# Optimization experiments

Hardware: AMD Instinct MI355X
Metric: run time of the kernel (lower is better)

The kernel has to match this reference:

```python
import math
import jax, jax.numpy as jnp
import numpy as np

B, T, C = 2, 2048, 1024
HEADS = 16
HD = C // HEADS  # 64


def setup_inputs() -> dict:
    key = jax.random.key(0)
    ks = jax.random.split(key, 5)
    s = 0.02
    return {
        "x": jax.random.normal(ks[0], (B, T, C), jnp.float32),
        "Wq": jax.random.normal(ks[1], (C, C), jnp.float32) * s,
        "bq": jnp.zeros((C,), jnp.float32),
        "Wk": jax.random.normal(ks[2], (C, HD), jnp.float32) * s,
        "bk": jnp.zeros((HD,), jnp.float32),
        "Wv": jax.random.normal(ks[3], (C, HD), jnp.float32) * s,
        "bv": jnp.zeros((HD,), jnp.float32),
        "Wo": jax.random.normal(ks[4], (C, C), jnp.float32) * s,
        "bo": jnp.zeros((C,), jnp.float32),
    }


def _rope_tables(seq_len, dim):
    pos = jnp.arange(seq_len, dtype=jnp.float32)
    freqs = 1.0 / (10000.0 ** (jnp.arange(0, dim, 2, dtype=jnp.float32) / dim))
    ang = pos[:, None] * freqs[None, :]          # (T, dim//2)
    # broadcast over (B, T, H, dim//2)
    return jnp.sin(ang)[None, :, None, :], jnp.cos(ang)[None, :, None, :]


def _apply_rope(t, sin, cos, dim):
    t1, t2 = t[..., : dim // 2], t[..., dim // 2 :]
    # matches torch source: emb[..., :d/2]=sin, emb[..., d/2:]=cos
    return jnp.concatenate([t1 * cos + t2 * sin, t1 * sin - t2 * cos], axis=-1)


def reference(x, Wq, bq, Wk, bk, Wv, bv, Wo, bo):
    Bx, Tx, Cx = x.shape
    q = (x @ Wq + bq).reshape(Bx, Tx, HEADS, HD)   # (B,T,H,hd)
    k = (x @ Wk + bk)[:, :, None, :]               # (B,T,1,hd) single KV head (MQA)
    v = (x @ Wv + bv)[:, :, None, :]
    sin, cos = _rope_tables(Tx, HD)
    q = _apply_rope(q, sin, cos, HD)
    k = _apply_rope(k, sin, cos, HD)
    att = jnp.einsum('bthd,bThd->bhtT', q, k) / math.sqrt(HD)
    causal = jnp.triu(jnp.ones((Tx, Tx), bool), 1)
    att = jnp.where(causal, -jnp.inf, att)
    att = jax.nn.softmax(att, axis=-1)
    out = jnp.einsum('bhtT,bThd->bthd', att, v).reshape(Bx, Tx, Cx)
    return out @ Wo + bo
```

## Files before the change

kernel.cpp:

```cpp
#include <hip/hip_runtime.h>
#include <math.h>

#define BSZ   2
#define TSEQ  2048
#define CDIM  1024
#define NHEAD 16
#define HDIM  64
#define BT    (BSZ*TSEQ)
#define NQKV  1152

typedef __attribute__((ext_vector_type(8))) short short8;
typedef __attribute__((ext_vector_type(4))) float f32x4;
typedef unsigned short u16;
typedef unsigned int   u32;

__device__ __forceinline__ u16 f2b(float f) {
    union { float f; u32 u; } c; c.f = f;
    u32 u = c.u;
    u += 0x7fffu + ((u >> 16) & 1u);
    return (u16)(u >> 16);
}
__device__ __forceinline__ u32 pack2(float lo, float hi) {
    return (u32)f2b(lo) | ((u32)f2b(hi) << 16);
}

__device__ __forceinline__ void async_copy16(const void* g, void* l) {
    __builtin_amdgcn_global_load_lds(
        (__attribute__((address_space(1))) const void*)g,
        (__attribute__((address_space(3))) void*)l,
        16, 0, 0);
}

__device__ __forceinline__ void transpose_tile(
    const float* __restrict__ W, u16* __restrict__ Wt,
    int K, int Nw, int nofs, int bx, int by, float (*T)[65])
{
    const int tid = threadIdx.x;
    const int k0 = by * 64, n0 = bx * 64;
    #pragma unroll
    for (int i = 0; i < 16; ++i) {
        int idx = i * 256 + tid, r = idx >> 6, c = idx & 63;
        T[r][c] = W[(size_t)(k0 + r) * Nw + n0 + c];
    }
    __syncthreads();
    #pragma unroll
    for (int i = 0; i < 16; ++i) {
        int idx = i * 256 + tid, rn = idx >> 6, ck = idx & 63;
        Wt[(size_t)(nofs + n0 + rn) * K + k0 + ck] = f2b(T[ck][rn]);
    }
}

__global__ __launch_bounds__(256) void prep_kernel(
    const float* __restrict__ x,
    const float* __restrict__ Wq, const float* __restrict__ Wk,
    const float* __restrict__ Wv, const float* __restrict__ Wo,
    const float* __restrict__ bq, const float* __restrict__ bk,
    const float* __restrict__ bv,
    u16* __restrict__ xb,
    u16* __restrict__ Wqkvt, u16* __restrict__ Wot, float* __restrict__ bqkv)
{
    __shared__ float T[64][65];
    const int bid = blockIdx.x;
    if (bid < 4096) {
        int i = bid * 256 + threadIdx.x;
        float4 f = ((const float4*)x)[i];
        u16* d = xb + (size_t)i * 4;
        d[0] = f2b(f.x); d[1] = f2b(f.y); d[2] = f2b(f.z); d[3] = f2b(f.w);
    } else if (bid < 4352) {
        int b2 = bid - 4096;
        transpose_tile(Wq, Wqkvt, 1024, 1024, 0, b2 & 15, b2 >> 4, T);
    } else if (bid < 4368) {
        transpose_tile(Wk, Wqkvt, 1024, 64, 1024, 0, bid - 4352, T);
    } else if (bid < 4384) {
        transpose_tile(Wv, Wqkvt, 1024, 64, 1088, 0, bid - 4368, T);
    } else if (bid < 4640) {
        int b2 = bid - 4384;
        transpose_tile(Wo, Wot, 1024, 1024, 0, b2 & 15, b2 >> 4, T);
    } else {
        for (int i = threadIdx.x; i < NQKV; i += 256)
            bqkv[i] = (i < 1024) ? bq[i] : (i < 1088 ? bk[i - 1024] : bv[i - 1088]);
    }
}

__global__ __launch_bounds__(256) void gemm_qkv_kernel(
    const u16* __restrict__ A, const u16* __restrict__ Bt,
    const float* __restrict__ bias,
    u16* __restrict__ qb, u16* __restrict__ kb, u16* __restrict__ vT)
{
    __shared__ __align__(16) u16 AsC[64 * 32];
    __shared__ __align__(16) u16 BsC[128 * 32];
    const int tid  = threadIdx.x;
    const int wave = tid >> 6, lane = tid & 63;
    const int ln16 = lane & 15, quad = lane >> 4;
    const int wm = wave >> 1, wn = wave & 1;
    const int m0 = blockIdx.y * 64, n0 = blockIdx.x * 128;
    const int K = CDIM;

    const int c_row = ((tid >> 6) << 4) + (tid & 15);
    const int c_k   = ((tid >> 4) & 3) * 8;
    const u16* ag  = &A [(size_t)(m0 + c_row)       * K + c_k];
    const u16* bg0 = &Bt[(size_t)(n0 + c_row)       * K + c_k];
    const u16* bg1 = &Bt[(size_t)(n0 + 64 + c_row)  * K + c_k];
    u16* a_l  = &AsC[(size_t)wave * 64 * 8];
    u16* b_l0 = &BsC[(size_t)wave * 64 * 8];
    u16* b_l1 = &BsC[(size_t)(wave + 4) * 64 * 8];

    f32x4 acc[2][4];
    #pragma unroll
    for (int i = 0; i < 2; ++i)
        #pragma unroll
        for (int j = 0; j < 4; ++j) acc[i][j] = (f32x4){0.f, 0.f, 0.f, 0.f};

    for (int k0 = 0; k0 < K; k0 += 32) {
        async_copy16(ag,  a_l);
        async_copy16(bg0, b_l0);
        async_copy16(bg1, b_l1);
        ag += 32; bg0 += 32; bg1 += 32;
        __syncthreads();

        short8 af[2], bf[4];
        #pragma unroll
        for (int mt = 0; mt < 2; ++mt)
            af[mt] = *(const short8*)&AsC[(((wm * 2 + mt) * 64) + quad * 16 + ln16) * 8];
        #pragma unroll
        for (int nt = 0; nt < 4; ++nt)
            bf[nt] = *(const short8*)&BsC[(((wn * 4 + nt) * 64) + quad * 16 + ln16) * 8];
        #pragma unroll
        for (int mt = 0; mt < 2; ++mt)
            #pragma unroll
            for (int nt = 0; nt < 4; ++nt)
                acc[mt][nt] = __builtin_amdgcn_mfma_f32_16x16x32_bf16(
                    af[mt], bf[nt], acc[mt][nt], 0, 0, 0);
        __syncthreads();
    }

    #pragma unroll
    for (int mt = 0; mt < 2; ++mt)
        #pragma unroll
        for (int nt = 0; nt < 4; ++nt) {
            float bb = bias[n0 + wn * 64 + nt * 16 + ln16];
            #pragma unroll
            for (int r = 0; r < 4; ++r) acc[mt][nt][r] += bb;
        }

    const int col0 = n0 + wn * 64;
    if (col0 < 1024) {
        const int hh = col0 >> 6;
        #pragma unroll
        for (int nt = 0; nt < 2; ++nt) {
            int j = nt * 16 + ln16;
            float fr = exp2f(-0.41524101186092029f * (float)j);
            #pragma unroll
            for (int mt = 0; mt < 2; ++mt)
                #pragma unroll
                for (int r = 0; r < 4; ++r) {
                    int m = m0 + wm * 32 + mt * 16 + quad * 4 + r;
                    float sn, cs;
                    __sincosf((float)(m & (TSEQ - 1)) * fr, &sn, &cs);
                    float t1 = acc[mt][nt][r], t2 = acc[mt][nt + 2][r];
                    u16* o = qb + (size_t)m * CDIM + hh * 64 + j;
                    o[0]  = f2b(fmaf(t1, cs,  t2 * sn) * 0.18033688011112043f);
                    o[32] = f2b(fmaf(t1, sn, -t2 * cs) * 0.18033688011112043f);
                }
        }
    } else if (wn == 0) {
        #pragma unroll
        for (int nt = 0; nt < 2; ++nt) {
            int j = nt * 16 + ln16;
            float fr = exp2f(-0.41524101186092029f * (float)j);
            #pragma unroll
            for (int mt = 0; mt < 2; ++mt)
                #pragma unroll
                for (int r = 0; r < 4; ++r) {
                    int m = m0 + wm * 32 + mt * 16 + quad * 4 + r;
                    float sn, cs;
                    __sincosf((float)(m & (TSEQ - 1)) * fr, &sn, &cs);
                    float t1 = acc[mt][nt][r], t2 = acc[mt][nt + 2][r];
                    u16* o = kb + (size_t)m * HDIM + j;
                    o[0]  = f2b(fmaf(t1, cs,  t2 * sn));
                    o[32] = f2b(fmaf(t1, sn, -t2 * cs));
                }
        }
    } else {
        #pragma unroll
        for (int nt = 0; nt < 4; ++nt) {
            int d = nt * 16 + ln16;
            #pragma unroll
            for (int mt = 0; mt < 2; ++mt) {
                int mr = m0 + wm * 32 + mt * 16 + quad * 4;
                int b  = mr >> 11, tq = mr & (TSEQ - 1);
                uint2 val;
                val.x = pack2(acc[mt][nt][0], acc[mt][nt][1]);
                val.y = pack2(acc[mt][nt][2], acc[mt][nt][3]);
                *(uint2*)&vT[(size_t)(b * HDIM + d) * TSEQ + tq] = val;
            }
        }
    }
}

__global__ __launch_bounds__(256) void gemm_mfma_kernel(
    const u16* __restrict__ A, const u16* __restrict__ Bt,
    const float* __restrict__ bias, float* __restrict__ Y,
    int M, int N, int K)
{
    __shared__ __align__(16) u16 AsC[64 * 32];
    __shared__ __align__(16) u16 BsC[128 * 32];
    const int tid  = threadIdx.x;
    const int wave = tid >> 6, lane = tid & 63;
    const int ln16 = lane & 15, quad = lane >> 4;
    const int wm = wave >> 1, wn = wave & 1;
    const int m0 = blockIdx.y * 64, n0 = blockIdx.x * 128;

    const int c_row = ((tid >> 6) << 4) + (tid & 15);
    const int c_k   = ((tid >> 4) & 3) * 8;
    const u16* ag  = &A [(size_t)(m0 + c_row)       * K + c_k];
    const u16* bg0 = &Bt[(size_t)(n0 + c_row)       * K + c_k];
    const u16* bg1 = &Bt[(size_t)(n0 + 64 + c_row)  * K + c_k];
    u16* a_l  = &AsC[(size_t)wave * 64 * 8];
    u16* b_l0 = &BsC[(size_t)wave * 64 * 8];
    u16* b_l1 = &BsC[(size_t)(wave + 4) * 64 * 8];

    f32x4 acc[2][4];
    #pragma unroll
    for (int i = 0; i < 2; ++i)
        #pragma unroll
        for (int j = 0; j < 4; ++j) acc[i][j] = (f32x4){0.f, 0.f, 0.f, 0.f};

    for (int k0 = 0; k0 < K; k0 += 32) {
        async_copy16(ag,  a_l);
        async_copy16(bg0, b_l0);
        async_copy16(bg1, b_l1);
        ag += 32; bg0 += 32; bg1 += 32;
        __syncthreads();

        short8 af[2], bf[4];
        #pragma unroll
        for (int mt = 0; mt < 2; ++mt)
            af[mt] = *(const short8*)&AsC[(((wm * 2 + mt) * 64) + quad * 16 + ln16) * 8];
        #pragma unroll
        for (int nt = 0; nt < 4; ++nt)
            bf[nt] = *(const short8*)&BsC[(((wn * 4 + nt) * 64) + quad * 16 + ln16) * 8];
        #pragma unroll
        for (int mt = 0; mt < 2; ++mt)
            #pragma unroll
            for (int nt = 0; nt < 4; ++nt)
                acc[mt][nt] = __builtin_amdgcn_mfma_f32_16x16x32_bf16(
                    af[mt], bf[nt], acc[mt][nt], 0, 0, 0);
        __syncthreads();
    }

    #pragma unroll
    for (int mt = 0; mt < 2; ++mt)
        #pragma unroll
        for (int nt = 0; nt < 4; ++nt) {
            int n = n0 + wn * 64 + nt * 16 + ln16;
            float bb = bias[n];
            #pragma unroll
            for (int r = 0; r < 4; ++r) {
                int m = m0 + wm * 32 + mt * 16 + quad * 4 + r;
                Y[(size_t)m * N + n] = acc[mt][nt][r] + bb;
            }
        }
}

__device__ __forceinline__ void flash_stage_kv(
    const u16* __restrict__ kb, const u16* __restrict__ vT,
    int b, int kt, u16* __restrict__ Ksb, u16* __restrict__ Vsb,
    const int* row_c, const int* off_c, int c0)
{
    const size_t kt0 = (size_t)(b * TSEQ + kt * 64);
    #pragma unroll
    for (int hf = 0; hf < 2; ++hf) {
        int cc = c0 + hf * 256;
        async_copy16(kb + (kt0 + row_c[hf]) * HDIM + off_c[hf], Ksb + cc * 8);
        async_copy16(vT + (size_t)(b * HDIM + row_c[hf]) * TSEQ + kt * 64 + off_c[hf],
                     Vsb + cc * 8);
    }
}

__device__ __forceinline__ void flash_tile(
    const u16* __restrict__ Ksb, const u16* __restrict__ Vsb,
    const u16* __restrict__ Qs, u16* __restrict__ Pw,
    int wave, int ln16, int quad, bool diag,
    float* lsum, f32x4* oacc)
{
    f32x4 sv[4];
    #pragma unroll
    for (int t = 0; t < 4; ++t) sv[t] = (f32x4){0.f, 0.f, 0.f, 0.f};
    #pragma unroll
    for (int kk2 = 0; kk2 < 2; ++kk2) {
        short8 af = *(const short8*)&Qs[(wave * 128 + kk2 * 64 + quad * 16 + ln16) * 8];
        #pragma unroll
        for (int t = 0; t < 4; ++t) {
            short8 bf = *(const short8*)&Ksb[(t * 128 + kk2 * 64 + quad * 16 + ln16) * 8];
            sv[t] = __builtin_amdgcn_mfma_f32_16x16x32_bf16(af, bf, sv[t], 0, 0, 0);
        }
    }

    if (diag) {
        #pragma unroll
        for (int t = 0; t < 4; ++t) {
            int key = t * 16 + ln16;
            #pragma unroll
            for (int r = 0; r < 4; ++r) {
                float e = (key > wave * 16 + quad * 4 + r) ? 0.f : exp2f(sv[t][r]);
                u32 bits = __float_as_uint(e);
                lsum[r] += __uint_as_float(bits & 0xffff0000u);
                Pw[(quad * 4 + r) * 72 + t * 16 + ln16] = (u16)(bits >> 16);
            }
        }
    } else {
        #pragma unroll
        for (int t = 0; t < 4; ++t)
            #pragma unroll
            for (int r = 0; r < 4; ++r) {
                float e = exp2f(sv[t][r]);
                u32 bits = __float_as_uint(e);
                lsum[r] += __uint_as_float(bits & 0xffff0000u);
                Pw[(quad * 4 + r) * 72 + t * 16 + ln16] = (u16)(bits >> 16);
            }
    }

    #pragma unroll
    for (int kk2 = 0; kk2 < 2; ++kk2) {
        short8 pf = *(const short8*)&Pw[ln16 * 72 + kk2 * 32 + quad * 8];
        #pragma unroll
        for (int t = 0; t < 4; ++t) {
            short8 vf = *(const short8*)&Vsb[(t * 128 + kk2 * 64 + quad * 16 + ln16) * 8];
            oacc[t] = __builtin_amdgcn_mfma_f32_16x16x32_bf16(pf, vf, oacc[t], 0, 0, 0);
        }
    }
}

__global__ __launch_bounds__(256) void flash_mfma_kernel(
    const u16* __restrict__ qb, const u16* __restrict__ kb,
    const u16* __restrict__ vT, u16* __restrict__ o)
{
    const int id  = blockIdx.x;
    const int qt  = 31 - (id >> 5);
    const int hb  = id & 31;
    const int h   = hb >> 1;
    const int b   = hb & 1;
    __shared__ __align__(16) u16 Qs [512 * 8];
    __shared__ __align__(16) u16 Ks0[512 * 8];
    __shared__ __align__(16) u16 Ks1[512 * 8];
    __shared__ __align__(16) u16 Vs0[512 * 8];
    __shared__ __align__(16) u16 Vs1[512 * 8];
    __shared__ __align__(16) u16 Ps[4 * 16 * 72];

    const int tid  = threadIdx.x;
    const int wave = tid >> 6, lane = tid & 63;
    const int ln16 = lane & 15, quad = lane >> 4;

    const int c0 = tid;
    int row_c[2], off_c[2];
    #pragma unroll
    for (int hf = 0; hf < 2; ++hf) {
        int c = c0 + hf * 256;
        row_c[hf] = ((c >> 7) << 4) | (c & 15);
        off_c[hf] = ((c >> 6) & 1) * 32 + ((c >> 4) & 3) * 8;
    }

    u16* Pw = &Ps[wave * 16 * 72];

    #pragma unroll
    for (int hf = 0; hf < 2; ++hf)
        async_copy16(
            qb + (size_t)(b * TSEQ + qt * 64 + row_c[hf]) * CDIM + h * HDIM + off_c[hf],
            Qs + (c0 + hf * 256) * 8);
    flash_stage_kv(kb, vT, b, 0, Ks0, Vs0, row_c, off_c, c0);

    float lsum[4];
    f32x4 oacc[4];
    #pragma unroll
    for (int r = 0; r < 4; ++r) lsum[r] = 0.f;
    #pragma unroll
    for (int t = 0; t < 4; ++t) oacc[t] = (f32x4){0.f, 0.f, 0.f, 0.f};

    int kt = 0;
    while (true) {
        __syncthreads();
        if (kt < qt) flash_stage_kv(kb, vT, b, kt + 1, Ks1, Vs1, row_c, off_c, c0);
        flash_tile(Ks0, Vs0, Qs, Pw, wave, ln16, quad, kt == qt, lsum, oacc);
        if (++kt > qt) break;
        __syncthreads();
        if (kt < qt) flash_stage_kv(kb, vT, b, kt + 1, Ks0, Vs0, row_c, off_c, c0);
        flash_tile(Ks1, Vs1, Qs, Pw, wave, ln16, quad, kt == qt, lsum, oacc);
        if (++kt > qt) break;
    }

    float inv[4];
    #pragma unroll
    for (int r = 0; r < 4; ++r) {
        float l = lsum[r];
        #pragma unroll
        for (int off = 1; off < 16; off <<= 1)
            l += __shfl_xor(l, off, 64);
        inv[r] = 1.0f / l;
    }
    #pragma unroll
    for (int t = 0; t < 4; ++t) {
        #pragma unroll
        for (int r = 0; r < 4; ++r) {
            int row = qt * 64 + wave * 16 + quad * 4 + r;
            int d   = t * 16 + ln16;
            o[(size_t)(b * TSEQ + row) * CDIM + h * HDIM + d] = f2b(oacc[t][r] * inv[r]);
        }
    }
}

extern "C" void kernel_launch(void* const* d_in, const int* in_sizes, int n_in,
                              void* d_out, int out_size, void* d_ws, size_t ws_size,
                              hipStream_t stream)
{
    const float* x  = (const float*)d_in[0];
    const float* Wq = (const float*)d_in[1];
    const float* bq = (const float*)d_in[2];
    const float* Wk = (const float*)d_in[3];
    const float* bk = (const float*)d_in[4];
    const float* Wv = (const float*)d_in[5];
    const float* bv = (const float*)d_in[6];
    const float* Wo = (const float*)d_in[7];
    const float* bo = (const float*)d_in[8];
    float* out = (float*)d_out;

    const size_t MB = 1u << 20;
    char* w = (char*)d_ws;
    u16*   xb   = (u16*)(w);
    u16*   aob  = (u16*)(w);
    u16*   qb   = (u16*)(w + 8 * MB);
    u16*   kb   = (u16*)(w + 16 * MB);
    u16*   vT   = (u16*)(w + 16 * MB + 512 * 1024);
    u16*   Wqkvt= (u16*)(w + 17 * MB);
    u16*   Wot  = (u16*)(w + 20 * MB);
    float* bqkv = (float*)(w + 22 * MB);

    prep_kernel<<<dim3(4641), dim3(256), 0, stream>>>(
        x, Wq, Wk, Wv, Wo, bq, bk, bv, xb, Wqkvt, Wot, bqkv);
    gemm_qkv_kernel<<<dim3(NQKV / 128, BT / 64), dim3(256), 0, stream>>>(
        xb, Wqkvt, bqkv, qb, kb, vT);
    flash_mfma_kernel<<<dim3(32 * NHEAD * BSZ), dim3(256), 0, stream>>>(
        qb, kb, vT, aob);
    gemm_mfma_kernel<<<dim3(CDIM / 128, BT / 64), dim3(256), 0, stream>>>(
        aob, Wot, bo, out, BT, CDIM, CDIM);
}
```

Before: 192.5 us.

## Enlarge GEMM tiles to 128x128 and pair causal query tiles per flash block

Both GEMM kernels now compute 128x128 output tiles per block, with each wave holding a 64x64 accumulator, which halves the grid and increases operand reuse from shared memory. The flash attention kernel now processes two query tiles per block, pid and 31-pid, so every block does the same amount of causal work and the grid is halved. The aim is better data reuse in the GEMMs and better load balance in attention. In exchange the GEMMs use more registers and run fewer blocks (288 and 256), which may leave the 256 CUs of the MI355X under-occupied, and attention now launches only 512 blocks.

```diff
diff --git a/kernel.cpp b/kernel.cpp
--- a/kernel.cpp
+++ b/kernel.cpp
@@ -87,46 +87,49 @@
     const float* __restrict__ bias,
     u16* __restrict__ qb, u16* __restrict__ kb, u16* __restrict__ vT)
 {
-    __shared__ __align__(16) u16 AsC[64 * 32];
+    __shared__ __align__(16) u16 AsC[128 * 32];
     __shared__ __align__(16) u16 BsC[128 * 32];
     const int tid  = threadIdx.x;
     const int wave = tid >> 6, lane = tid & 63;
     const int ln16 = lane & 15, quad = lane >> 4;
     const int wm = wave >> 1, wn = wave & 1;
-    const int m0 = blockIdx.y * 64, n0 = blockIdx.x * 128;
+    const int m0 = blockIdx.y * 128, n0 = blockIdx.x * 128;
     const int K = CDIM;
 
-    const int c_row = ((tid >> 6) << 4) + (tid & 15);
-    const int c_k   = ((tid >> 4) & 3) * 8;
-    const u16* ag  = &A [(size_t)(m0 + c_row)       * K + c_k];
+    const int c_row = (wave << 4) + ln16;
+    const int c_k   = quad * 8;
+    const u16* ag0 = &A [(size_t)(m0 + c_row)       * K + c_k];
+    const u16* ag1 = &A [(size_t)(m0 + 64 + c_row)  * K + c_k];
     const u16* bg0 = &Bt[(size_t)(n0 + c_row)       * K + c_k];
     const u16* bg1 = &Bt[(size_t)(n0 + 64 + c_row)  * K + c_k];
-    u16* a_l  = &AsC[(size_t)wave * 64 * 8];
+    u16* a_l0 = &AsC[(size_t)wave * 64 * 8];
+    u16* a_l1 = &AsC[(size_t)(wave + 4) * 64 * 8];
     u16* b_l0 = &BsC[(size_t)wave * 64 * 8];
     u16* b_l1 = &BsC[(size_t)(wave + 4) * 64 * 8];
 
-    f32x4 acc[2][4];
-    #pragma unroll
-    for (int i = 0; i < 2; ++i)
+    f32x4 acc[4][4];
+    #pragma unroll
+    for (int i = 0; i < 4; ++i)
         #pragma unroll
         for (int j = 0; j < 4; ++j) acc[i][j] = (f32x4){0.f, 0.f, 0.f, 0.f};
 
     for (int k0 = 0; k0 < K; k0 += 32) {
-        async_copy16(ag,  a_l);
+        async_copy16(ag0, a_l0);
+        async_copy16(ag1, a_l1);
         async_copy16(bg0, b_l0);
         async_copy16(bg1, b_l1);
-        ag += 32; bg0 += 32; bg1 += 32;
+        ag0 += 32; ag1 += 32; bg0 += 32; bg1 += 32;
         __syncthreads();
 
-        short8 af[2], bf[4];
-        #pragma unroll
-        for (int mt = 0; mt < 2; ++mt)
-            af[mt] = *(const short8*)&AsC[(((wm * 2 + mt) * 64) + quad * 16 + ln16) * 8];
+        short8 af[4], bf[4];
+        #pragma unroll
+        for (int mt = 0; mt < 4; ++mt)
+            af[mt] = *(const short8*)&AsC[(((wm * 4 + mt) * 64) + quad * 16 + ln16) * 8];
         #pragma unroll
         for (int nt = 0; nt < 4; ++nt)
             bf[nt] = *(const short8*)&BsC[(((wn * 4 + nt) * 64) + quad * 16 + ln16) * 8];
         #pragma unroll
-        for (int mt = 0; mt < 2; ++mt)
+        for (int mt = 0; mt < 4; ++mt)
             #pragma unroll
             for (int nt = 0; nt < 4; ++nt)
                 acc[mt][nt] = __builtin_amdgcn_mfma_f32_16x16x32_bf16(
@@ -135,7 +138,7 @@
     }
 
     #pragma unroll
-    for (int mt = 0; mt < 2; ++mt)
+    for (int mt = 0; mt < 4; ++mt)
         #pragma unroll
         for (int nt = 0; nt < 4; ++nt) {
             float bb = bias[n0 + wn * 64 + nt * 16 + ln16];
@@ -151,10 +154,10 @@
             int j = nt * 16 + ln16;
             float fr = exp2f(-0.41524101186092029f * (float)j);
             #pragma unroll
-            for (int mt = 0; mt < 2; ++mt)
+            for (int mt = 0; mt < 4; ++mt)
                 #pragma unroll
                 for (int r = 0; r < 4; ++r) {
-                    int m = m0 + wm * 32 + mt * 16 + quad * 4 + r;
+                    int m = m0 + wm * 64 + mt * 16 + quad * 4 + r;
                     float sn, cs;
                     __sincosf((float)(m & (TSEQ - 1)) * fr, &sn, &cs);
                     float t1 = acc[mt][nt][r], t2 = acc[mt][nt + 2][r];
@@ -169,10 +172,10 @@
             int j = nt * 16 + ln16;
             float fr = exp2f(-0.41524101186092029f * (float)j);
             #pragma unroll
-            for (int mt = 0; mt < 2; ++mt)
+            for (int mt = 0; mt < 4; ++mt)
                 #pragma unroll
                 for (int r = 0; r < 4; ++r) {
-                    int m = m0 + wm * 32 + mt * 16 + quad * 4 + r;
+                    int m = m0 + wm * 64 + mt * 16 + quad * 4 + r;
                     float sn, cs;
                     __sincosf((float)(m & (TSEQ - 1)) * fr, &sn, &cs);
                     float t1 = acc[mt][nt][r], t2 = acc[mt][nt + 2][r];
@@ -186,8 +189,8 @@
         for (int nt = 0; nt < 4; ++nt) {
             int d = nt * 16 + ln16;
             #pragma unroll
-            for (int mt = 0; mt < 2; ++mt) {
-                int mr = m0 + wm * 32 + mt * 16 + quad * 4;
+            for (int mt = 0; mt < 4; ++mt) {
+                int mr = m0 + wm * 64 + mt * 16 + quad * 4;
                 int b  = mr >> 11, tq = mr & (TSEQ - 1);
                 uint2 val;
                 val.x = pack2(acc[mt][nt][0], acc[mt][nt][1]);
@@ -203,45 +206,48 @@
     const float* __restrict__ bias, float* __restrict__ Y,
     int M, int N, int K)
 {
-    __shared__ __align__(16) u16 AsC[64 * 32];
+    __shared__ __align__(16) u16 AsC[128 * 32];
     __shared__ __align__(16) u16 BsC[128 * 32];
     const int tid  = threadIdx.x;
     const int wave = tid >> 6, lane = tid & 63;
     const int ln16 = lane & 15, quad = lane >> 4;
     const int wm = wave >> 1, wn = wave & 1;
-    const int m0 = blockIdx.y * 64, n0 = blockIdx.x * 128;
-
-    const int c_row = ((tid >> 6) << 4) + (tid & 15);
-    const int c_k   = ((tid >> 4) & 3) * 8;
-    const u16* ag  = &A [(size_t)(m0 + c_row)       * K + c_k];
+    const int m0 = blockIdx.y * 128, n0 = blockIdx.x * 128;
+
+    const int c_row = (wave << 4) + ln16;
+    const int c_k   = quad * 8;
+    const u16* ag0 = &A [(size_t)(m0 + c_row)       * K + c_k];
+    const u16* ag1 = &A [(size_t)(m0 + 64 + c_row)  * K + c_k];
     const u16* bg0 = &Bt[(size_t)(n0 + c_row)       * K + c_k];
     const u16* bg1 = &Bt[(size_t)(n0 + 64 + c_row)  * K + c_k];
-    u16* a_l  = &AsC[(size_t)wave * 64 * 8];
+    u16* a_l0 = &AsC[(size_t)wave * 64 * 8];
+    u16* a_l1 = &AsC[(size_t)(wave + 4) * 64 * 8];
     u16* b_l0 = &BsC[(size_t)wave * 64 * 8];
     u16* b_l1 = &BsC[(size_t)(wave + 4) * 64 * 8];
 
-    f32x4 acc[2][4];
-    #pragma unroll
-    for (int i = 0; i < 2; ++i)
+    f32x4 acc[4][4];
+    #pragma unroll
+    for (int i = 0; i < 4; ++i)
         #pragma unroll
         for (int j = 0; j < 4; ++j) acc[i][j] = (f32x4){0.f, 0.f, 0.f, 0.f};
 
     for (int k0 = 0; k0 < K; k0 += 32) {
-        async_copy16(ag,  a_l);
+        async_copy16(ag0, a_l0);
+        async_copy16(ag1, a_l1);
         async_copy16(bg0, b_l0);
         async_copy16(bg1, b_l1);
-        ag += 32; bg0 += 32; bg1 += 32;
+        ag0 += 32; ag1 += 32; bg0 += 32; bg1 += 32;
         __syncthreads();
 
-        short8 af[2], bf[4];
-        #pragma unroll
-        for (int mt = 0; mt < 2; ++mt)
-            af[mt] = *(const short8*)&AsC[(((wm * 2 + mt) * 64) + quad * 16 + ln16) * 8];
+        short8 af[4], bf[4];
+        #pragma unroll
+        for (int mt = 0; mt < 4; ++mt)
+            af[mt] = *(const short8*)&AsC[(((wm * 4 + mt) * 64) + quad * 16 + ln16) * 8];
         #pragma unroll
         for (int nt = 0; nt < 4; ++nt)
             bf[nt] = *(const short8*)&BsC[(((wn * 4 + nt) * 64) + quad * 16 + ln16) * 8];
         #pragma unroll
-        for (int mt = 0; mt < 2; ++mt)
+        for (int mt = 0; mt < 4; ++mt)
             #pragma unroll
             for (int nt = 0; nt < 4; ++nt)
                 acc[mt][nt] = __builtin_amdgcn_mfma_f32_16x16x32_bf16(
@@ -250,14 +256,14 @@
     }
 
     #pragma unroll
-    for (int mt = 0; mt < 2; ++mt)
+    for (int mt = 0; mt < 4; ++mt)
         #pragma unroll
         for (int nt = 0; nt < 4; ++nt) {
             int n = n0 + wn * 64 + nt * 16 + ln16;
             float bb = bias[n];
             #pragma unroll
             for (int r = 0; r < 4; ++r) {
-                int m = m0 + wm * 32 + mt * 16 + quad * 4 + r;
+                int m = m0 + wm * 64 + mt * 16 + quad * 4 + r;
                 Y[(size_t)m * N + n] = acc[mt][nt][r] + bb;
             }
         }
@@ -337,7 +343,7 @@
     const u16* __restrict__ vT, u16* __restrict__ o)
 {
     const int id  = blockIdx.x;
-    const int qt  = 31 - (id >> 5);
+    const int pid = id >> 5;
     const int hb  = id & 31;
     const int h   = hb >> 1;
     const int b   = hb & 1;
@@ -363,48 +369,54 @@
 
     u16* Pw = &Ps[wave * 16 * 72];
 
-    #pragma unroll
-    for (int hf = 0; hf < 2; ++hf)
-        async_copy16(
-            qb + (size_t)(b * TSEQ + qt * 64 + row_c[hf]) * CDIM + h * HDIM + off_c[hf],
-            Qs + (c0 + hf * 256) * 8);
-    flash_stage_kv(kb, vT, b, 0, Ks0, Vs0, row_c, off_c, c0);
-
-    float lsum[4];
-    f32x4 oacc[4];
-    #pragma unroll
-    for (int r = 0; r < 4; ++r) lsum[r] = 0.f;
-    #pragma unroll
-    for (int t = 0; t < 4; ++t) oacc[t] = (f32x4){0.f, 0.f, 0.f, 0.f};
-
-    int kt = 0;
-    while (true) {
-        __syncthreads();
-        if (kt < qt) flash_stage_kv(kb, vT, b, kt + 1, Ks1, Vs1, row_c, off_c, c0);
-        flash_tile(Ks0, Vs0, Qs, Pw, wave, ln16, quad, kt == qt, lsum, oacc);
-        if (++kt > qt) break;
-        __syncthreads();
-        if (kt < qt) flash_stage_kv(kb, vT, b, kt + 1, Ks0, Vs0, row_c, off_c, c0);
-        flash_tile(Ks1, Vs1, Qs, Pw, wave, ln16, quad, kt == qt, lsum, oacc);
-        if (++kt > qt) break;
-    }
-
-    float inv[4];
-    #pragma unroll
-    for (int r = 0; r < 4; ++r) {
-        float l = lsum[r];
-        #pragma unroll
-        for (int off = 1; off < 16; off <<= 1)
-            l += __shfl_xor(l, off, 64);
-        inv[r] = 1.0f / l;
-    }
-    #pragma unroll
-    for (int t = 0; t < 4; ++t) {
+    #pragma unroll 1
+    for (int ph = 0; ph < 2; ++ph) {
+        const int qt = ph ? (31 - pid) : pid;
+        if (ph) __syncthreads();
+
+        #pragma unroll
+        for (int hf = 0; hf < 2; ++hf)
+            async_copy16(
+                qb + (size_t)(b * TSEQ + qt * 64 + row_c[hf]) * CDIM + h * HDIM + off_c[hf],
+                Qs + (c0 + hf * 256) * 8);
+        flash_stage_kv(kb, vT, b, 0, Ks0, Vs0, row_c, off_c, c0);
+
+        float lsum[4];
+        f32x4 oacc[4];
+        #pragma unroll
+        for (int r = 0; r < 4; ++r) lsum[r] = 0.f;
+        #pragma unroll
+        for (int t = 0; t < 4; ++t) oacc[t] = (f32x4){0.f, 0.f, 0.f, 0.f};
+
+        int kt = 0;
+        while (true) {
+            __syncthreads();
+            if (kt < qt) flash_stage_kv(kb, vT, b, kt + 1, Ks1, Vs1, row_c, off_c, c0);
+            flash_tile(Ks0, Vs0, Qs, Pw, wave, ln16, quad, kt == qt, lsum, oacc);
+            if (++kt > qt) break;
+            __syncthreads();
+            if (kt < qt) flash_stage_kv(kb, vT, b, kt + 1, Ks0, Vs0, row_c, off_c, c0);
+            flash_tile(Ks1, Vs1, Qs, Pw, wave, ln16, quad, kt == qt, lsum, oacc);
+            if (++kt > qt) break;
+        }
+
+        float inv[4];
         #pragma unroll
         for (int r = 0; r < 4; ++r) {
-            int row = qt * 64 + wave * 16 + quad * 4 + r;
-            int d   = t * 16 + ln16;
-            o[(size_t)(b * TSEQ + row) * CDIM + h * HDIM + d] = f2b(oacc[t][r] * inv[r]);
+            float l = lsum[r];
+            #pragma unroll
+            for (int off = 1; off < 16; off <<= 1)
+                l += __shfl_xor(l, off, 64);
+            inv[r] = 1.0f / l;
+        }
+        #pragma unroll
+        for (int t = 0; t < 4; ++t) {
+            #pragma unroll
+            for (int r = 0; r < 4; ++r) {
+                int row = qt * 64 + wave * 16 + quad * 4 + r;
+                int d   = t * 16 + ln16;
+                o[(size_t)(b * TSEQ + row) * CDIM + h * HDIM + d] = f2b(oacc[t][r] * inv[r]);
+            }
         }
     }
 }
@@ -437,10 +449,10 @@
 
     prep_kernel<<<dim3(4641), dim3(256), 0, stream>>>(
         x, Wq, Wk, Wv, Wo, bq, bk, bv, xb, Wqkvt, Wot, bqkv);
-    gemm_qkv_kernel<<<dim3(NQKV / 128, BT / 64), dim3(256), 0, stream>>>(
+    gemm_qkv_kernel<<<dim3(NQKV / 128, BT / 128), dim3(256), 0, stream>>>(
         xb, Wqkvt, bqkv, qb, kb, vT);
-    flash_mfma_kernel<<<dim3(32 * NHEAD * BSZ), dim3(256), 0, stream>>>(
+    flash_mfma_kernel<<<dim3(16 * NHEAD * BSZ), dim3(256), 0, stream>>>(
         qb, kb, vT, aob);
-    gemm_mfma_kernel<<<dim3(CDIM / 128, BT / 64), dim3(256), 0, stream>>>(
+    gemm_mfma_kernel<<<dim3(CDIM / 128, BT / 128), dim3(256), 0, stream>>>(
         aob, Wot, bo, out, BT, CDIM, CDIM);
 }
```

Result: slower. 202.7 us (+5.3%).

## Enlarge flash query tile to 128 rows, pair causal tiles, MFMA row sums

Applied to the files above, without the earlier changes.

The attention kernel now processes 128 query rows per block (32 per wave, two 16-row MFMA tiles), so each staged K/V tile is reused across twice as many queries. Each block handles a pair of query tiles (pr and 15-pr) in sequence to balance causal work, and the grid shrinks to 256 blocks. Row sums of P are now computed with an MFMA against a ones vector instead of scalar adds plus shuffles, and V fragments are kept in registers across both row tiles. This raises register pressure and LDS use, and the smaller grid may underfill the GPU's compute units.

```diff
diff --git a/kernel.cpp b/kernel.cpp
--- a/kernel.cpp
+++ b/kernel.cpp
@@ -278,56 +278,73 @@
     }
 }
 
-__device__ __forceinline__ void flash_tile(
+__device__ __forceinline__ void flash_tile128(
     const u16* __restrict__ Ksb, const u16* __restrict__ Vsb,
     const u16* __restrict__ Qs, u16* __restrict__ Pw,
-    int wave, int ln16, int quad, bool diag,
-    float* lsum, f32x4* oacc)
-{
-    f32x4 sv[4];
-    #pragma unroll
-    for (int t = 0; t < 4; ++t) sv[t] = (f32x4){0.f, 0.f, 0.f, 0.f};
+    int wave, int ln16, int quad, int rbase, int kbase,
+    f32x4* lacc, f32x4 (*oacc)[4])
+{
+    if (kbase >= rbase + 32) return;
+    const bool diag = (kbase + 63 > rbase);
+
+    f32x4 sv[2][4];
+    #pragma unroll
+    for (int mt = 0; mt < 2; ++mt)
+        #pragma unroll
+        for (int t = 0; t < 4; ++t) sv[mt][t] = (f32x4){0.f, 0.f, 0.f, 0.f};
     #pragma unroll
     for (int kk2 = 0; kk2 < 2; ++kk2) {
-        short8 af = *(const short8*)&Qs[(wave * 128 + kk2 * 64 + quad * 16 + ln16) * 8];
+        short8 af0 = *(const short8*)&Qs[((wave * 2 + 0) * 128 + kk2 * 64 + quad * 16 + ln16) * 8];
+        short8 af1 = *(const short8*)&Qs[((wave * 2 + 1) * 128 + kk2 * 64 + quad * 16 + ln16) * 8];
         #pragma unroll
         for (int t = 0; t < 4; ++t) {
             short8 bf = *(const short8*)&Ksb[(t * 128 + kk2 * 64 + quad * 16 + ln16) * 8];
-            sv[t] = __builtin_amdgcn_mfma_f32_16x16x32_bf16(af, bf, sv[t], 0, 0, 0);
-        }
-    }
-
-    if (diag) {
-        #pragma unroll
-        for (int t = 0; t < 4; ++t) {
-            int key = t * 16 + ln16;
-            #pragma unroll
-            for (int r = 0; r < 4; ++r) {
-                float e = (key > wave * 16 + quad * 4 + r) ? 0.f : exp2f(sv[t][r]);
-                u32 bits = __float_as_uint(e);
-                lsum[r] += __uint_as_float(bits & 0xffff0000u);
-                Pw[(quad * 4 + r) * 72 + t * 16 + ln16] = (u16)(bits >> 16);
+            sv[0][t] = __builtin_amdgcn_mfma_f32_16x16x32_bf16(af0, bf, sv[0][t], 0, 0, 0);
+            sv[1][t] = __builtin_amdgcn_mfma_f32_16x16x32_bf16(af1, bf, sv[1][t], 0, 0, 0);
+        }
+    }
+
+    const short8 ones = {0x3F80, 0x3F80, 0x3F80, 0x3F80,
+                         0x3F80, 0x3F80, 0x3F80, 0x3F80};
+    short8 vreg[8];
+
+    #pragma unroll
+    for (int mt = 0; mt < 2; ++mt) {
+        if (diag) {
+            #pragma unroll
+            for (int t = 0; t < 4; ++t) {
+                int key = kbase + t * 16 + ln16;
+                #pragma unroll
+                for (int r = 0; r < 4; ++r) {
+                    int row = rbase + mt * 16 + quad * 4 + r;
+                    float e = (key > row) ? 0.f : exp2f(sv[mt][t][r]);
+                    Pw[(quad * 4 + r) * 72 + t * 16 + ln16] =
+                        (u16)(__float_as_uint(e) >> 16);
+                }
             }
-        }
-    } else {
-        #pragma unroll
-        for (int t = 0; t < 4; ++t)
-            #pragma unroll
-            for (int r = 0; r < 4; ++r) {
-                float e = exp2f(sv[t][r]);
-                u32 bits = __float_as_uint(e);
-                lsum[r] += __uint_as_float(bits & 0xffff0000u);
-                Pw[(quad * 4 + r) * 72 + t * 16 + ln16] = (u16)(bits >> 16);
+        } else {
+            #pragma unroll
+            for (int t = 0; t < 4; ++t)
+                #pragma unroll
+                for (int r = 0; r < 4; ++r) {
+                    float e = exp2f(sv[mt][t][r]);
+                    Pw[(quad * 4 + r) * 72 + t * 16 + ln16] =
+                        (u16)(__float_as_uint(e) >> 16);
+                }
+        }
+
+        #pragma unroll
+        for (int kk2 = 0; kk2 < 2; ++kk2) {
+            short8 pf = *(const short8*)&Pw[ln16 * 72 + kk2 * 32 + quad * 8];
+            lacc[mt] = __builtin_amdgcn_mfma_f32_16x16x32_bf16(pf, ones, lacc[mt], 0, 0, 0);
+            #pragma unroll
+            for (int t = 0; t < 4; ++t) {
+                if (mt == 0)
+                    vreg[kk2 * 4 + t] =
+                        *(const short8*)&Vsb[(t * 128 + kk2 * 64 + quad * 16 + ln16) * 8];
+                oacc[mt][t] = __builtin_amdgcn_mfma_f32_16x16x32_bf16(
+                    pf, vreg[kk2 * 4 + t], oacc[mt][t], 0, 0, 0);
             }
-    }
-
-    #pragma unroll
-    for (int kk2 = 0; kk2 < 2; ++kk2) {
-        short8 pf = *(const short8*)&Pw[ln16 * 72 + kk2 * 32 + quad * 8];
-        #pragma unroll
-        for (int t = 0; t < 4; ++t) {
-            short8 vf = *(const short8*)&Vsb[(t * 128 + kk2 * 64 + quad * 16 + ln16) * 8];
-            oacc[t] = __builtin_amdgcn_mfma_f32_16x16x32_bf16(pf, vf, oacc[t], 0, 0, 0);
         }
     }
 }
@@ -337,11 +354,11 @@
     const u16* __restrict__ vT, u16* __restrict__ o)
 {
     const int id  = blockIdx.x;
-    const int qt  = 31 - (id >> 5);
+    const int pr  = id >> 5;
     const int hb  = id & 31;
     const int h   = hb >> 1;
     const int b   = hb & 1;
-    __shared__ __align__(16) u16 Qs [512 * 8];
+    __shared__ __align__(16) u16 Qs [1024 * 8];
     __shared__ __align__(16) u16 Ks0[512 * 8];
     __shared__ __align__(16) u16 Ks1[512 * 8];
     __shared__ __align__(16) u16 Vs0[512 * 8];
@@ -363,49 +380,63 @@
 
     u16* Pw = &Ps[wave * 16 * 72];
 
-    #pragma unroll
-    for (int hf = 0; hf < 2; ++hf)
-        async_copy16(
-            qb + (size_t)(b * TSEQ + qt * 64 + row_c[hf]) * CDIM + h * HDIM + off_c[hf],
-            Qs + (c0 + hf * 256) * 8);
-    flash_stage_kv(kb, vT, b, 0, Ks0, Vs0, row_c, off_c, c0);
-
-    float lsum[4];
-    f32x4 oacc[4];
-    #pragma unroll
-    for (int r = 0; r < 4; ++r) lsum[r] = 0.f;
-    #pragma unroll
-    for (int t = 0; t < 4; ++t) oacc[t] = (f32x4){0.f, 0.f, 0.f, 0.f};
-
-    int kt = 0;
-    while (true) {
-        __syncthreads();
-        if (kt < qt) flash_stage_kv(kb, vT, b, kt + 1, Ks1, Vs1, row_c, off_c, c0);
-        flash_tile(Ks0, Vs0, Qs, Pw, wave, ln16, quad, kt == qt, lsum, oacc);
-        if (++kt > qt) break;
-        __syncthreads();
-        if (kt < qt) flash_stage_kv(kb, vT, b, kt + 1, Ks0, Vs0, row_c, off_c, c0);
-        flash_tile(Ks1, Vs1, Qs, Pw, wave, ln16, quad, kt == qt, lsum, oacc);
-        if (++kt > qt) break;
-    }
-
-    float inv[4];
-    #pragma unroll
-    for (int r = 0; r < 4; ++r) {
-        float l = lsum[r];
-        #pragma unroll
-        for (int off = 1; off < 16; off <<= 1)
-            l += __shfl_xor(l, off, 64);
-        inv[r] = 1.0f / l;
-    }
-    #pragma unroll
-    for (int t = 0; t < 4; ++t) {
+    #pragma unroll 1
+    for (int ph = 0; ph < 2; ++ph) {
+        const int qt = ph ? (15 - pr) : pr;
+        const int nt = 2 * qt + 2;
+        if (ph) __syncthreads();
+
+        #pragma unroll
+        for (int cc = 0; cc < 4; ++cc) {
+            int c  = c0 + cc * 256;
+            int rw = ((c >> 7) << 4) | (c & 15);
+            int of = ((c >> 6) & 1) * 32 + ((c >> 4) & 3) * 8;
+            async_copy16(
+                qb + (size_t)(b * TSEQ + qt * 128 + rw) * CDIM + h * HDIM + of,
+                Qs + (size_t)c * 8);
+        }
+        flash_stage_kv(kb, vT, b, 0, Ks0, Vs0, row_c, off_c, c0);
+
+        f32x4 lacc[2];
+        f32x4 oacc[2][4];
+        #pragma unroll
+        for (int mt = 0; mt < 2; ++mt) {
+            lacc[mt] = (f32x4){0.f, 0.f, 0.f, 0.f};
+            #pragma unroll
+            for (int t = 0; t < 4; ++t) oacc[mt][t] = (f32x4){0.f, 0.f, 0.f, 0.f};
+        }
+
+        const int rbase = qt * 128 + wave * 32;
+
+        int kt = 0;
+        while (true) {
+            __syncthreads();
+            if (kt + 1 < nt) flash_stage_kv(kb, vT, b, kt + 1, Ks1, Vs1, row_c, off_c, c0);
+            flash_tile128(Ks0, Vs0, Qs, Pw, wave, ln16, quad, rbase, kt * 64, lacc, oacc);
+            if (++kt >= nt) break;
+            __syncthreads();
+            if (kt + 1 < nt) flash_stage_kv(kb, vT, b, kt + 1, Ks0, Vs0, row_c, off_c, c0);
+            flash_tile128(Ks1, Vs1, Qs, Pw, wave, ln16, quad, rbase, kt * 64, lacc, oacc);
+            if (++kt >= nt) break;
+        }
+
+        float inv0[4], inv1[4];
         #pragma unroll
         for (int r = 0; r < 4; ++r) {
-            int row = qt * 64 + wave * 16 + quad * 4 + r;
-            int d   = t * 16 + ln16;
-            o[(size_t)(b * TSEQ + row) * CDIM + h * HDIM + d] = f2b(oacc[t][r] * inv[r]);
-        }
+            inv0[r] = 1.0f / lacc[0][r];
+            inv1[r] = 1.0f / lacc[1][r];
+        }
+        #pragma unroll
+        for (int mt = 0; mt < 2; ++mt)
+            #pragma unroll
+            for (int t = 0; t < 4; ++t)
+                #pragma unroll
+                for (int r = 0; r < 4; ++r) {
+                    int row = rbase + mt * 16 + quad * 4 + r;
+                    int d   = t * 16 + ln16;
+                    o[(size_t)(b * TSEQ + row) * CDIM + h * HDIM + d] =
+                        f2b(oacc[mt][t][r] * (mt ? inv1[r] : inv0[r]));
+                }
     }
 }
 
@@ -439,7 +470,7 @@
         x, Wq, Wk, Wv, Wo, bq, bk, bv, xb, Wqkvt, Wot, bqkv);
     gemm_qkv_kernel<<<dim3(NQKV / 128, BT / 64), dim3(256), 0, stream>>>(
         xb, Wqkvt, bqkv, qb, kb, vT);
-    flash_mfma_kernel<<<dim3(32 * NHEAD * BSZ), dim3(256), 0, stream>>>(
+    flash_mfma_kernel<<<dim3(8 * NHEAD * BSZ), dim3(256), 0, stream>>>(
         qb, kb, vT, aob);
     gemm_mfma_kernel<<<dim3(CDIM / 128, BT / 64), dim3(256), 0, stream>>>(
         aob, Wot, bo, out, BT, CDIM, CDIM);
```

Result: slower. 207.8 us (+7.9%).

## Double-buffer GEMM LDS tiles and compute softmax row sums via MFMA

Applied to the files above, without the earlier changes.

Both GEMM kernels switch to two LDS buffers, so the async copy of the next K-slice is issued before the MFMA work on the current slice, removing one barrier per step. The flash kernel stops accumulating per-lane row sums with scalar adds and shuffle reductions. It instead multiplies the bf16 P tile by a ones vector through an extra MFMA, which gives the row sum directly. This adds LDS usage and one MFMA per half-tile, in exchange for fewer VALU ops and no final cross-lane reduction.

```diff
diff --git a/kernel.cpp b/kernel.cpp
--- a/kernel.cpp
+++ b/kernel.cpp
@@ -82,13 +82,32 @@
     }
 }
 
+__device__ __forceinline__ void gemm_step(
+    const u16* __restrict__ As, const u16* __restrict__ Bs,
+    int wm, int wn, int quad, int ln16, f32x4 (*acc)[4])
+{
+    short8 af[2], bf[4];
+    #pragma unroll
+    for (int mt = 0; mt < 2; ++mt)
+        af[mt] = *(const short8*)&As[(((wm * 2 + mt) * 64) + quad * 16 + ln16) * 8];
+    #pragma unroll
+    for (int nt = 0; nt < 4; ++nt)
+        bf[nt] = *(const short8*)&Bs[(((wn * 4 + nt) * 64) + quad * 16 + ln16) * 8];
+    #pragma unroll
+    for (int mt = 0; mt < 2; ++mt)
+        #pragma unroll
+        for (int nt = 0; nt < 4; ++nt)
+            acc[mt][nt] = __builtin_amdgcn_mfma_f32_16x16x32_bf16(
+                af[mt], bf[nt], acc[mt][nt], 0, 0, 0);
+}
+
 __global__ __launch_bounds__(256) void gemm_qkv_kernel(
     const u16* __restrict__ A, const u16* __restrict__ Bt,
     const float* __restrict__ bias,
     u16* __restrict__ qb, u16* __restrict__ kb, u16* __restrict__ vT)
 {
-    __shared__ __align__(16) u16 AsC[64 * 32];
-    __shared__ __align__(16) u16 BsC[128 * 32];
+    __shared__ __align__(16) u16 AsC[2][64 * 32];
+    __shared__ __align__(16) u16 BsC[2][128 * 32];
     const int tid  = threadIdx.x;
     const int wave = tid >> 6, lane = tid & 63;
     const int ln16 = lane & 15, quad = lane >> 4;
@@ -101,9 +120,9 @@
     const u16* ag  = &A [(size_t)(m0 + c_row)       * K + c_k];
     const u16* bg0 = &Bt[(size_t)(n0 + c_row)       * K + c_k];
     const u16* bg1 = &Bt[(size_t)(n0 + 64 + c_row)  * K + c_k];
-    u16* a_l  = &AsC[(size_t)wave * 64 * 8];
-    u16* b_l0 = &BsC[(size_t)wave * 64 * 8];
-    u16* b_l1 = &BsC[(size_t)(wave + 4) * 64 * 8];
+    u16* a_l [2] = { &AsC[0][(size_t)wave * 64 * 8],       &AsC[1][(size_t)wave * 64 * 8] };
+    u16* b_l0[2] = { &BsC[0][(size_t)wave * 64 * 8],       &BsC[1][(size_t)wave * 64 * 8] };
+    u16* b_l1[2] = { &BsC[0][(size_t)(wave + 4) * 64 * 8], &BsC[1][(size_t)(wave + 4) * 64 * 8] };
 
     f32x4 acc[2][4];
     #pragma unroll
@@ -111,27 +130,23 @@
         #pragma unroll
         for (int j = 0; j < 4; ++j) acc[i][j] = (f32x4){0.f, 0.f, 0.f, 0.f};
 
-    for (int k0 = 0; k0 < K; k0 += 32) {
-        async_copy16(ag,  a_l);
-        async_copy16(bg0, b_l0);
-        async_copy16(bg1, b_l1);
-        ag += 32; bg0 += 32; bg1 += 32;
-        __syncthreads();
-
-        short8 af[2], bf[4];
-        #pragma unroll
-        for (int mt = 0; mt < 2; ++mt)
-            af[mt] = *(const short8*)&AsC[(((wm * 2 + mt) * 64) + quad * 16 + ln16) * 8];
-        #pragma unroll
-        for (int nt = 0; nt < 4; ++nt)
-            bf[nt] = *(const short8*)&BsC[(((wn * 4 + nt) * 64) + quad * 16 + ln16) * 8];
-        #pragma unroll
-        for (int mt = 0; mt < 2; ++mt)
-            #pragma unroll
-            for (int nt = 0; nt < 4; ++nt)
-                acc[mt][nt] = __builtin_amdgcn_mfma_f32_16x16x32_bf16(
-                    af[mt], bf[nt], acc[mt][nt], 0, 0, 0);
-        __syncthreads();
+    async_copy16(ag, a_l[0]); async_copy16(bg0, b_l0[0]); async_copy16(bg1, b_l1[0]);
+    __syncthreads();
+
+    for (int k0 = 0; k0 < K; k0 += 64) {
+        async_copy16(ag + 32, a_l[1]);
+        async_copy16(bg0 + 32, b_l0[1]);
+        async_copy16(bg1 + 32, b_l1[1]);
+        gemm_step(AsC[0], BsC[0], wm, wn, quad, ln16, acc);
+        __syncthreads();
+        if (k0 + 64 < K) {
+            async_copy16(ag + 64, a_l[0]);
+            async_copy16(bg0 + 64, b_l0[0]);
+            async_copy16(bg1 + 64, b_l1[0]);
+        }
+        gemm_step(AsC[1], BsC[1], wm, wn, quad, ln16, acc);
+        __syncthreads();
+        ag += 64; bg0 += 64; bg1 += 64;
     }
 
     #pragma unroll
@@ -203,8 +218,8 @@
     const float* __restrict__ bias, float* __restrict__ Y,
     int M, int N, int K)
 {
-    __shared__ __align__(16) u16 AsC[64 * 32];
-    __shared__ __align__(16) u16 BsC[128 * 32];
+    __shared__ __align__(16) u16 AsC[2][64 * 32];
+    __shared__ __align__(16) u16 BsC[2][128 * 32];
     const int tid  = threadIdx.x;
     const int wave = tid >> 6, lane = tid & 63;
     const int ln16 = lane & 15, quad = lane >> 4;
@@ -216,9 +231,9 @@
     const u16* ag  = &A [(size_t)(m0 + c_row)       * K + c_k];
     const u16* bg0 = &Bt[(size_t)(n0 + c_row)       * K + c_k];
     const u16* bg1 = &Bt[(size_t)(n0 + 64 + c_row)  * K + c_k];
-    u16* a_l  = &AsC[(size_t)wave * 64 * 8];
-    u16* b_l0 = &BsC[(size_t)wave * 64 * 8];
-    u16* b_l1 = &BsC[(size_t)(wave + 4) * 64 * 8];
+    u16* a_l [2] = { &AsC[0][(size_t)wave * 64 * 8],       &AsC[1][(size_t)wave * 64 * 8] };
+    u16* b_l0[2] = { &BsC[0][(size_t)wave * 64 * 8],       &BsC[1][(size_t)wave * 64 * 8] };
+    u16* b_l1[2] = { &BsC[0][(size_t)(wave + 4) * 64 * 8], &BsC[1][(size_t)(wave + 4) * 64 * 8] };
 
     f32x4 acc[2][4];
     #pragma unroll
@@ -226,27 +241,23 @@
         #pragma unroll
         for (int j = 0; j < 4; ++j) acc[i][j] = (f32x4){0.f, 0.f, 0.f, 0.f};
 
-    for (int k0 = 0; k0 < K; k0 += 32) {
-        async_copy16(ag,  a_l);
-        async_copy16(bg0, b_l0);
-        async_copy16(bg1, b_l1);
-        ag += 32; bg0 += 32; bg1 += 32;
-        __syncthreads();
-
-        short8 af[2], bf[4];
-        #pragma unroll
-        for (int mt = 0; mt < 2; ++mt)
-            af[mt] = *(const short8*)&AsC[(((wm * 2 + mt) * 64) + quad * 16 + ln16) * 8];
-        #pragma unroll
-        for (int nt = 0; nt < 4; ++nt)
-            bf[nt] = *(const short8*)&BsC[(((wn * 4 + nt) * 64) + quad * 16 + ln16) * 8];
-        #pragma unroll
-        for (int mt = 0; mt < 2; ++mt)
-            #pragma unroll
-            for (int nt = 0; nt < 4; ++nt)
-                acc[mt][nt] = __builtin_amdgcn_mfma_f32_16x16x32_bf16(
-                    af[mt], bf[nt], acc[mt][nt], 0, 0, 0);
-        __syncthreads();
+    async_copy16(ag, a_l[0]); async_copy16(bg0, b_l0[0]); async_copy16(bg1, b_l1[0]);
+    __syncthreads();
+
+    for (int k0 = 0; k0 < K; k0 += 64) {
+        async_copy16(ag + 32, a_l[1]);
+        async_copy16(bg0 + 32, b_l0[1]);
+        async_copy16(bg1 + 32, b_l1[1]);
+        gemm_step(AsC[0], BsC[0], wm, wn, quad, ln16, acc);
+        __syncthreads();
+        if (k0 + 64 < K) {
+            async_copy16(ag + 64, a_l[0]);
+            async_copy16(bg0 + 64, b_l0[0]);
+            async_copy16(bg1 + 64, b_l1[0]);
+        }
+        gemm_step(AsC[1], BsC[1], wm, wn, quad, ln16, acc);
+        __syncthreads();
+        ag += 64; bg0 += 64; bg1 += 64;
     }
 
     #pragma unroll
@@ -282,7 +293,7 @@
     const u16* __restrict__ Ksb, const u16* __restrict__ Vsb,
     const u16* __restrict__ Qs, u16* __restrict__ Pw,
     int wave, int ln16, int quad, bool diag,
-    float* lsum, f32x4* oacc)
+    f32x4* lacc, f32x4* oacc)
 {
     f32x4 sv[4];
     #pragma unroll
@@ -304,9 +315,8 @@
             #pragma unroll
             for (int r = 0; r < 4; ++r) {
                 float e = (key > wave * 16 + quad * 4 + r) ? 0.f : exp2f(sv[t][r]);
-                u32 bits = __float_as_uint(e);
-                lsum[r] += __uint_as_float(bits & 0xffff0000u);
-                Pw[(quad * 4 + r) * 72 + t * 16 + ln16] = (u16)(bits >> 16);
+                Pw[(quad * 4 + r) * 72 + t * 16 + ln16] =
+                    (u16)(__float_as_uint(e) >> 16);
             }
         }
     } else {
@@ -315,15 +325,17 @@
             #pragma unroll
             for (int r = 0; r < 4; ++r) {
                 float e = exp2f(sv[t][r]);
-                u32 bits = __float_as_uint(e);
-                lsum[r] += __uint_as_float(bits & 0xffff0000u);
-                Pw[(quad * 4 + r) * 72 + t * 16 + ln16] = (u16)(bits >> 16);
+                Pw[(quad * 4 + r) * 72 + t * 16 + ln16] =
+                    (u16)(__float_as_uint(e) >> 16);
             }
     }
 
+    const short8 ones = {0x3F80, 0x3F80, 0x3F80, 0x3F80,
+                         0x3F80, 0x3F80, 0x3F80, 0x3F80};
     #pragma unroll
     for (int kk2 = 0; kk2 < 2; ++kk2) {
         short8 pf = *(const short8*)&Pw[ln16 * 72 + kk2 * 32 + quad * 8];
+        *lacc = __builtin_amdgcn_mfma_f32_16x16x32_bf16(pf, ones, *lacc, 0, 0, 0);
         #pragma unroll
         for (int t = 0; t < 4; ++t) {
             short8 vf = *(const short8*)&Vsb[(t * 128 + kk2 * 64 + quad * 16 + ln16) * 8];
@@ -370,10 +382,8 @@
             Qs + (c0 + hf * 256) * 8);
     flash_stage_kv(kb, vT, b, 0, Ks0, Vs0, row_c, off_c, c0);
 
-    float lsum[4];
+    f32x4 lacc = (f32x4){0.f, 0.f, 0.f, 0.f};
     f32x4 oacc[4];
-    #pragma unroll
-    for (int r = 0; r < 4; ++r) lsum[r] = 0.f;
     #pragma unroll
     for (int t = 0; t < 4; ++t) oacc[t] = (f32x4){0.f, 0.f, 0.f, 0.f};
 
@@ -381,23 +391,17 @@
     while (true) {
         __syncthreads();
         if (kt < qt) flash_stage_kv(kb, vT, b, kt + 1, Ks1, Vs1, row_c, off_c, c0);
-        flash_tile(Ks0, Vs0, Qs, Pw, wave, ln16, quad, kt == qt, lsum, oacc);
+        flash_tile(Ks0, Vs0, Qs, Pw, wave, ln16, quad, kt == qt, &lacc, oacc);
         if (++kt > qt) break;
         __syncthreads();
         if (kt < qt) flash_stage_kv(kb, vT, b, kt + 1, Ks0, Vs0, row_c, off_c, c0);
-        flash_tile(Ks1, Vs1, Qs, Pw, wave, ln16, quad, kt == qt, lsum, oacc);
+        flash_tile(Ks1, Vs1, Qs, Pw, wave, ln16, quad, kt == qt, &lacc, oacc);
         if (++kt > qt) break;
     }
 
     float inv[4];
     #pragma unroll
-    for (int r = 0; r < 4; ++r) {
-        float l = lsum[r];
-        #pragma unroll
-        for (int off = 1; off < 16; off <<= 1)
-            l += __shfl_xor(l, off, 64);
-        inv[r] = 1.0f / l;
-    }
+    for (int r = 0; r < 4; ++r) inv[r] = 1.0f / lacc[r];
     #pragma unroll
     for (int t = 0; t < 4; ++t) {
         #pragma unroll
```

After: 193.6 us. Within noise of the previous version (+0.6%).
